# Kernel optimization log

Measured on AMD Instinct MI355X. Metric: run time of the kernel, lower is better.

Reference implementation:

```python
import jax, jax.numpy as jnp
import numpy as np

EPS = 1e-5

def _sqnorm(x):
    return jnp.sum(x * x, axis=-1, keepdims=True)

def _norm(x):
    return jnp.sqrt(_sqnorm(x) + 1e-15)

def _artanh(x):
    return jnp.arctanh(jnp.clip(x, -1.0 + EPS, 1.0 - EPS))

def exp0(v):
    n = _norm(v)
    return jnp.tanh(n) * v / jnp.maximum(n, EPS)

def log0(x):
    n = jnp.clip(_norm(x), EPS, 1.0 - EPS)
    return _artanh(n) * x / n

def mob_scalar(x, r):
    n = jnp.clip(_norm(x), EPS, 1.0 - EPS)
    return jnp.tanh(r * _artanh(n)) * x / n

def mob_add(x, y):
    x2 = _sqnorm(x); y2 = _sqnorm(y)
    xy = jnp.sum(x * y, axis=-1, keepdims=True)
    num = (1.0 + 2.0 * xy + y2) * x + (1.0 - x2) * y
    den = 1.0 + 2.0 * xy + x2 * y2
    return num / jnp.maximum(den, EPS)

def pdist(x, y):
    # Poincare-ball geodesic distance, keepdims on last axis
    d2 = _sqnorm(x - y)
    den = jnp.maximum((1.0 - _sqnorm(x)) * (1.0 - _sqnorm(y)), EPS)
    return jnp.arccosh(jnp.maximum(1.0 + 2.0 * d2 / den, 1.0 + 1e-7))

def _coattention(D, Q, q1):
    # vectorized form of the per-slot loop: each slot i reads the ORIGINAL D[:, i]
    Dd = jax.lax.stop_gradient(D)                       # Zk_s is detached in torch
    # [N, F_D, F_Q, 1] attention over Q neighbors for every D slot
    G = jax.nn.softmax(-pdist(Dd[:, :, None, :], Q[:, None, :, :]), axis=2)
    nh = exp0(jnp.sum(log0(mob_scalar(Q[:, None, :, :], G)), axis=2))  # [N, F_D, d]
    return mob_add(mob_scalar(Dd, q1), nh)

def _aggregate(h_self, h_neigh, scalar):
    att = jax.nn.softmax(-pdist(h_self[:, None, :], h_neigh), axis=1)  # [N, F, 1]
    nTE = exp0(jnp.sum(log0(mob_scalar(h_neigh, att)), axis=1))        # [N, d]
    return mob_add(mob_scalar(h_self, scalar), nTE)

def _mode_forward(x, D_idx, Q_idx, emb0, emb1, win, bin_, q, qq, q1, aw1, ab1, aw2, wout, bout):
    f = jnp.concatenate([emb0[x[:, 0]], emb1[x[:, 1]]], axis=-1)  # [N, 64]
    f = exp0(f @ win + bin_)
    D = f[D_idx]; Q = f[Q_idx]                                    # [N, F, d]
    h_neigh = _coattention(D, Q, q1)
    e1 = _aggregate(f, h_neigh, q)
    e2 = _aggregate(f, Q, qq)
    z = jnp.stack([log0(e1), log0(e2)], axis=1)                   # [N, 2, d]
    beta = jax.nn.softmax(jnp.tanh(z @ aw1 + ab1) @ aw2, axis=1)  # [N, 2, 1]
    rst = exp0(jnp.sum(beta * z, axis=1))
    return exp0(log0(rst) @ wout + bout)

N, F, DH, V0, V1 = 2048, 20, 64, 100000, 1000

def setup_inputs() -> dict:
    key = jax.random.key(0)
    ks = jax.random.split(key, 32)
    def mk(k, shape, s=0.1):
        return (jax.random.normal(k, shape) * s).astype(jnp.float32)
    inp = {
        'x': jax.random.randint(ks[0], (N, 2), 0, V1).astype(jnp.int32),
        'idx_sim': jax.random.randint(ks[1], (N, F), 0, N).astype(jnp.int32),
        'idx_cor': jax.random.randint(ks[2], (N, F), 0, N).astype(jnp.int32),
    }
    for mi, m in enumerate(['sim', 'cor']):
        kk = jax.random.split(ks[3 + mi], 12)
        inp[f'emb0_{m}'] = mk(kk[0], (V0, 32))
        inp[f'emb1_{m}'] = mk(kk[1], (V1, 32))
        inp[f'win_{m}'] = mk(kk[2], (64, DH))
        inp[f'bin_{m}'] = mk(kk[3], (DH,))
        inp[f'q_{m}'] = jnp.full((1,), 0.1, jnp.float32)
        inp[f'qq_{m}'] = jnp.full((1,), 0.1, jnp.float32)
        inp[f'q1_{m}'] = jnp.full((1,), 0.1, jnp.float32)
        inp[f'aw1_{m}'] = mk(kk[4], (64, 32))
        inp[f'ab1_{m}'] = mk(kk[5], (32,))
        inp[f'aw2_{m}'] = mk(kk[6], (32, 1))
        inp[f'wout_{m}'] = mk(kk[7], (DH, 64))
        inp[f'bout_{m}'] = mk(kk[8], (64,))
    return inp

def reference(x, idx_sim, idx_cor,
              emb0_sim, emb1_sim, win_sim, bin_sim, q_sim, qq_sim, q1_sim,
              aw1_sim, ab1_sim, aw2_sim, wout_sim, bout_sim,
              emb0_cor, emb1_cor, win_cor, bin_cor, q_cor, qq_cor, q1_cor,
              aw1_cor, ab1_cor, aw2_cor, wout_cor, bout_cor):
    # mode 'sim': D = feat[idx_cor], Q = feat[idx_sim]; mode 'cor': swapped
    out_sim = _mode_forward(x, idx_cor, idx_sim, emb0_sim, emb1_sim, win_sim, bin_sim,
                            q_sim, qq_sim, q1_sim, aw1_sim, ab1_sim, aw2_sim, wout_sim, bout_sim)
    out_cor = _mode_forward(x, idx_sim, idx_cor, emb0_cor, emb1_cor, win_cor, bin_cor,
                            q_cor, qq_cor, q1_cor, aw1_cor, ab1_cor, aw2_cor, wout_cor, bout_cor)
    return jnp.stack([out_sim, out_cor], axis=0)  # [2, N, 64]
```

## Files before the change

### kernel.cpp

```cpp
#include <hip/hip_runtime.h>

#define EPS 1e-5f
#define ONE_M_EPS (1.0f - 1e-5f)
#define NROW 2048
#define FF 20
#define DH 64
#define PADW (DH + 4)
#define PADH 72
#define NPAIR (FF * FF)
#define NPAIR2 (NPAIR + FF)

typedef float v2f __attribute__((ext_vector_type(2)));
typedef _Float16 v2h __attribute__((ext_vector_type(2)));

__device__ __forceinline__ float frcp(float x) { return __builtin_amdgcn_rcpf(x); }
__device__ __forceinline__ float fsq(float x) { return __builtin_amdgcn_sqrtf(x); }
__device__ __forceinline__ v2f pkfma(v2f a, v2f b, v2f c) {
  return __builtin_elementwise_fma(a, b, c);
}
__device__ __forceinline__ float rdlane(float v, int lane) {
  return __int_as_float(__builtin_amdgcn_readlane(__float_as_int(v), lane));
}

template <int CTRL>
__device__ __forceinline__ float dppadd(float x) {
  int t = __builtin_amdgcn_update_dpp(0, __float_as_int(x), CTRL, 0xf, 0xf, false);
  return x + __int_as_float(t);
}
__device__ __forceinline__ float wredb(float v) {
  v = dppadd<0x111>(v);
  v = dppadd<0x112>(v);
  v = dppadd<0x114>(v);
  v = dppadd<0x118>(v);
  v = dppadd<0x142>(v);
  v = dppadd<0x143>(v);
  return rdlane(v, 63);
}

__device__ __forceinline__ float ftanh(float x) {
  float ax = fabsf(x);
  float e = __expf(-2.f * ax);
  float t = (1.f - e) * frcp(1.f + e);
  return copysignf(t, x);
}

__device__ __forceinline__ float ftanhp(float x) {
  float e = __expf(-2.f * x);
  return (1.f - e) * frcp(1.f + e);
}

__device__ __forceinline__ float fatanh(float x) {
  return 0.5f * __logf((1.f + x) * frcp(1.f - x));
}

__device__ __forceinline__ float clampn(float x) {
  return fminf(fmaxf(x, EPS), ONE_M_EPS);
}

__device__ __forceinline__ float expnacosh(float arg) {
  return frcp(arg + fsq(fmaxf(arg * arg - 1.f, 0.f)));
}

__device__ __forceinline__ float dot64(const float* __restrict__ a,
                                       const float* __restrict__ b) {
  const float4* ap = (const float4*)a;
  const float4* bp = (const float4*)b;
  v2f accA = {0.f, 0.f}, accB = {0.f, 0.f};
#pragma unroll
  for (int kk = 0; kk < DH / 4; ++kk) {
    float4 x = ap[kk];
    float4 y = bp[kk];
    accA = pkfma(v2f{x.x, x.y}, v2f{y.x, y.y}, accA);
    accB = pkfma(v2f{x.z, x.w}, v2f{y.z, y.w}, accB);
  }
  v2f acc = accA + accB;
  return acc.x + acc.y;
}

__device__ __forceinline__ float dot64h(const _Float16* __restrict__ a,
                                        const _Float16* __restrict__ b) {
  const uint4* ap = (const uint4*)a;
  const uint4* bp = (const uint4*)b;
  float acc0 = 0.f, acc1 = 0.f;
#pragma unroll
  for (int kk = 0; kk < 8; ++kk) {
    uint4 x = ap[kk];
    uint4 y = bp[kk];
    acc0 = __builtin_amdgcn_fdot2(__builtin_bit_cast(v2h, x.x),
                                  __builtin_bit_cast(v2h, y.x), acc0, false);
    acc1 = __builtin_amdgcn_fdot2(__builtin_bit_cast(v2h, x.y),
                                  __builtin_bit_cast(v2h, y.y), acc1, false);
    acc0 = __builtin_amdgcn_fdot2(__builtin_bit_cast(v2h, x.z),
                                  __builtin_bit_cast(v2h, y.z), acc0, false);
    acc1 = __builtin_amdgcn_fdot2(__builtin_bit_cast(v2h, x.w),
                                  __builtin_bit_cast(v2h, y.w), acc1, false);
  }
  return acc0 + acc1;
}

struct FeatParams {
  const float *emb0, *emb1, *win, *bin;
  float* fout;
};

struct ModeParams {
  const float* f;
  const int *Didx, *Qidx;
  const float *q1p, *qp, *qqp, *aw1, *ab1, *aw2, *wout, *bout;
  float* out;
};

__global__ __launch_bounds__(64) void feat_kernel(const int* __restrict__ x,
                                                  FeatParams ps, FeatParams pc) {
  const int bid = blockIdx.x;
  const int mode = bid >= NROW;
  const FeatParams P = mode ? pc : ps;
  const int n = bid - mode * NROW;
  const int l = threadIdx.x;
  __shared__ float u[DH];
  int x0 = x[n * 2 + 0];
  int x1 = x[n * 2 + 1];
  u[l] = (l < 32) ? P.emb0[x0 * 32 + l] : P.emb1[x1 * 32 + (l - 32)];
  __syncthreads();
  v2f acc2 = {P.bin[l], 0.f};
#pragma unroll
  for (int k = 0; k < DH; k += 2) {
    v2f uv = *(const v2f*)&u[k];
    v2f wv = {P.win[k * DH + l], P.win[(k + 1) * DH + l]};
    acc2 = pkfma(uv, wv, acc2);
  }
  float acc = acc2.x + acc2.y;
  float a2 = wredb(acc * acc);
  float nn = fsq(a2 + 1e-15f);
  P.fout[n * DH + l] = ftanhp(nn) * frcp(fmaxf(nn, EPS)) * acc;
}

__global__ __launch_bounds__(256) void mode_kernel(ModeParams pm0,
                                                   ModeParams pm1) {
  const int bid = blockIdx.x;
  const int mode = bid >= NROW;
  const ModeParams P = mode ? pm1 : pm0;
  const int n = bid - mode * NROW;
  const int tid = threadIdx.x;
  const int l = tid & 63;
  const int w = tid >> 6;

  __shared__ alignas(16) float Ds[FF][PADW];
  __shared__ alignas(16) float Qs[FF][PADW];
  __shared__ alignas(16) float fs_[PADW];
  __shared__ alignas(16) _Float16 Dh[FF][PADH];
  __shared__ alignas(16) _Float16 Qh[FF][PADH];
  __shared__ alignas(16) _Float16 fh[PADH];
  __shared__ alignas(16) float Gm[NPAIR];
  __shared__ float Fq[FF];
  __shared__ float D2[FF];
  __shared__ float FD[FF], X2s[FF];
  __shared__ float Q2[FF], WQ[FF];
  __shared__ float C1[FF], C2[FF], WH[FF];
  __shared__ float zb[2][DH];
  __shared__ float ub[DH];

  float (*As)[PADW] = Qs;

  const float* f = P.f;
  float fv = f[n * DH + l];

  for (int i = w; i < FF; i += 4) {
    float dv = f[P.Didx[n * FF + i] * DH + l];
    float qv = f[P.Qidx[n * FF + i] * DH + l];
    Ds[i][l] = dv;
    Qs[i][l] = qv;
    Dh[i][l] = (_Float16)dv;
    Qh[i][l] = (_Float16)qv;
  }
  if (w == 0) {
    fs_[l] = fv;
    fh[l] = (_Float16)fv;
  }
  float f2 = wredb(fv * fv);
  float fnc = clampn(fsq(f2 + 1e-15f));
  float fA = fatanh(fnc);
  float q1 = P.q1p[0], qsc = P.qp[0], qqsc = P.qqp[0];
  __syncthreads();

  if (w < 2 && l < FF) {
    const float* rp = (w == 0) ? &Ds[l][0] : &Qs[l][0];
    float dot = dot64(rp, rp);
    float nc = clampn(fsq(dot + 1e-15f));
    float at = fatanh(nc);
    if (w == 0) {
      D2[l] = dot;
      float fd = ftanh(q1 * at) * frcp(nc);
      FD[l] = fd;
      X2s[l] = fd * fd * dot;
    } else {
      Q2[l] = dot;
      WQ[l] = at * frcp(nc);
    }
  }
  __syncthreads();

  float qregS[FF];
#pragma unroll
  for (int j = 0; j < FF; ++j) qregS[j] = WQ[j] * Qs[j][l];

  for (int p = tid; p < NPAIR2; p += 256) {
    int i = p / FF;
    int j = p - i * FF;
    const _Float16* ap = (i < FF) ? &Dh[i][0] : &fh[0];
    float dot = dot64h(ap, &Qh[j][0]);
    if (i < FF) {
      float d2 = D2[i] + Q2[j] - 2.f * dot;
      float den = fmaxf((1.f - D2[i]) * (1.f - Q2[j]), EPS);
      float arg = fmaxf(1.f + 2.f * d2 * frcp(den), 1.f + 1e-7f);
      Gm[p] = expnacosh(arg);
    } else {
      Fq[j] = dot;
    }
  }
  __syncthreads();

  float acc5[5];
#pragma unroll
  for (int s = 0; s < 5; ++s) {
    const int i = w + 4 * s;
    const float4* gr = (const float4*)(&Gm[i * FF]);
    v2f ss2 = {0.f, 0.f};
    v2f ac2 = {0.f, 0.f};
#pragma unroll
    for (int jq = 0; jq < FF / 4; ++jq) {
      float4 g4 = gr[jq];
      ss2 += v2f{g4.x, g4.y} + v2f{g4.z, g4.w};
      ac2 = pkfma(v2f{g4.x, g4.y}, v2f{qregS[4 * jq + 0], qregS[4 * jq + 1]},
                  ac2);
      ac2 = pkfma(v2f{g4.z, g4.w}, v2f{qregS[4 * jq + 2], qregS[4 * jq + 3]},
                  ac2);
    }
    float acc = (ac2.x + ac2.y) * frcp(ss2.x + ss2.y);
    acc5[s] = acc;
    As[i][l] = acc;
  }
  __syncthreads();

  if (w == 0) {
    const bool isA = (l < FF);
    const bool isX = (l >= 32 && l < 32 + FF);
    const float* pa = isA ? &As[l][0] : (isX ? &As[l - 32][0] : &fs_[0]);
    const float* pc2 = isA ? &As[l][0] : (isX ? &Ds[l - 32][0] : &fs_[0]);
    float dotv = dot64(pa, pc2);
    float xyv = __shfl(dotv, l + 32, 64);
    if (isA) {
      float a2 = dotv;
      float xy0 = xyv;
      float nn = fsq(a2 + 1e-15f);
      float ec = ftanhp(nn) * frcp(fmaxf(nn, EPS));
      float fDc = FD[l];
      float x2 = X2s[l];
      float y2 = ec * ec * a2;
      float xy = fDc * ec * xy0;
      float al = 1.f + 2.f * xy + y2;
      float be = 1.f - x2;
      float rd = frcp(fmaxf(1.f + 2.f * xy + x2 * y2, EPS));
      C1[l] = al * fDc * rd;
      C2[l] = be * ec * rd;
      float h2 = (al * al * x2 + 2.f * al * be * xy + be * be * y2) * rd * rd;
      D2[l] = h2;
      float nc = clampn(fsq(h2 + 1e-15f));
      WH[l] = fatanh(nc) * frcp(nc);
    }
  }
  __syncthreads();

#pragma unroll
  for (int s = 0; s < 5; ++s) {
    const int i = w + 4 * s;
    Ds[i][l] = fmaf(C1[i], Ds[i][l], C2[i] * acc5[s]);
  }
  __syncthreads();

  if (w < 2) {
    float a1 = 0.f;
    float wh = 1.f;
    if (w == 0) {
      if (l < FF) {
        float h2 = D2[l];
        wh = WH[l];
        float dot = dot64(&fs_[0], &Ds[l][0]);
        float d2 = f2 + h2 - 2.f * dot;
        float den = fmaxf((1.f - f2) * (1.f - h2), EPS);
        float arg = fmaxf(1.f + 2.f * d2 * frcp(den), 1.f + 1e-7f);
        a1 = expnacosh(arg);
      }
    } else {
      if (l < FF) {
        float d2 = f2 + Q2[l] - 2.f * Fq[l];
        float den = fmaxf((1.f - f2) * (1.f - Q2[l]), EPS);
        float arg = fmaxf(1.f + 2.f * d2 * frcp(den), 1.f + 1e-7f);
        a1 = expnacosh(arg);
      }
    }
    float s = wredb(a1);
    float c = (l < FF) ? a1 * frcp(s) * wh : 0.f;
    float accE = 0.f;
    if (w == 0) {
#pragma unroll
      for (int j = 0; j < FF; ++j) accE = fmaf(rdlane(c, j), Ds[j][l], accE);
    } else {
#pragma unroll
      for (int j = 0; j < FF; ++j) accE = fmaf(rdlane(c, j), qregS[j], accE);
    }
    float a2 = wredb(accE * accE);
    float nn = fsq(a2 + 1e-15f);
    float ec = ftanhp(nn) * frcp(fmaxf(nn, EPS));
    float nTE = ec * accE;
    float r = (w == 0) ? qsc : qqsc;
    float fsc = ftanh(r * fA) * frcp(fnc);
    float xv = fsc * fv;
    float x2 = fsc * fsc * f2;
    float y2 = ec * ec * a2;
    float xy = wredb(xv * nTE);
    float al = 1.f + 2.f * xy + y2;
    float be = 1.f - x2;
    float rd = frcp(fmaxf(1.f + 2.f * xy + x2 * y2, EPS));
    float ev = (al * xv + be * nTE) * rd;
    float es = (al * al * x2 + 2.f * al * be * xy + be * be * y2) * rd * rd;
    float n1 = clampn(fsq(es + 1e-15f));
    zb[w][l] = fatanh(n1) * frcp(n1) * ev;
  }
  __syncthreads();

  if (w == 0) {
    int p_ = l >> 5, c_ = l & 31;
    v2f mm2 = {P.ab1[c_], 0.f};
#pragma unroll
    for (int k = 0; k < DH; k += 2) {
      v2f zv = *(const v2f*)&zb[p_][k];
      v2f av = {P.aw1[k * 32 + c_], P.aw1[(k + 1) * 32 + c_]};
      mm2 = pkfma(zv, av, mm2);
    }
    float tt = ftanh(mm2.x + mm2.y);
    float sr = tt * P.aw2[c_];
    sr = dppadd<0x111>(sr);
    sr = dppadd<0x112>(sr);
    sr = dppadd<0x114>(sr);
    sr = dppadd<0x118>(sr);
    sr = dppadd<0x142>(sr);
    float s0 = rdlane(sr, 31);
    float s1 = rdlane(sr, 63);
    float bm = fmaxf(s0, s1);
    float b0 = __expf(s0 - bm), b1 = __expf(s1 - bm);
    float bi = frcp(b0 + b1);
    b0 *= bi;
    b1 *= bi;
    float rv = fmaf(b0, zb[0][l], b1 * zb[1][l]);
    float r2 = wredb(rv * rv);
    float rn = fsq(r2 + 1e-15f);
    float sc = ftanhp(rn) * frcp(fmaxf(rn, EPS));
    float rst = sc * rv;
    float rr = sc * sc * r2;
    float rc = clampn(fsq(rr + 1e-15f));
    ub[l] = fatanh(rc) * frcp(rc) * rst;
  }
  __syncthreads();

  if (w == 0) {
    v2f oo2 = {0.f, 0.f};
#pragma unroll
    for (int k = 0; k < DH; k += 2) {
      v2f uv = *(const v2f*)&ub[k];
      v2f wv = {P.wout[k * DH + l], P.wout[(k + 1) * DH + l]};
      oo2 = pkfma(uv, wv, oo2);
    }
    float oo = P.bout[l] + oo2.x + oo2.y;
    float o2 = wredb(oo * oo);
    float on = fsq(o2 + 1e-15f);
    P.out[n * DH + l] = ftanhp(on) * frcp(fmaxf(on, EPS)) * oo;
  }
}

extern "C" void kernel_launch(void* const* d_in, const int* in_sizes, int n_in,
                              void* d_out, int out_size, void* d_ws,
                              size_t ws_size, hipStream_t stream) {
  const int* x = (const int*)d_in[0];
  const int* idx_sim = (const int*)d_in[1];
  const int* idx_cor = (const int*)d_in[2];
  const float* p[2][12];
  for (int m = 0; m < 2; ++m)
    for (int k = 0; k < 12; ++k) p[m][k] = (const float*)d_in[3 + m * 12 + k];

  float* fsim = (float*)d_ws;
  float* fcor = fsim + NROW * DH;
  float* out = (float*)d_out;

  FeatParams fps = {p[0][0], p[0][1], p[0][2], p[0][3], fsim};
  FeatParams fpc = {p[1][0], p[1][1], p[1][2], p[1][3], fcor};
  feat_kernel<<<2 * NROW, 64, 0, stream>>>(x, fps, fpc);

  ModeParams m0 = {fsim, idx_cor, idx_sim, p[0][6], p[0][4], p[0][5],
                   p[0][7], p[0][8], p[0][9], p[0][10], p[0][11], out};
  ModeParams m1 = {fcor, idx_sim, idx_cor, p[1][6], p[1][4], p[1][5],
                   p[1][7], p[1][8], p[1][9], p[1][10], p[1][11], out + NROW * DH};
  mode_kernel<<<2 * NROW, 256, 0, stream>>>(m0, m1);
}
```

Before: 41.82 us.

## Store gathered neighbor rows only as fp16 and use fp16 dots for norms

Drops the fp32 shared copies of the D and Q neighbor rows and keeps only fp16 copies. Norms, the attention-output dots and Q register loads now read the fp16 data, and the coattention result is written to a new fp16 buffer. The mob_add cross term is computed from an unscaled dot that is issued right after the norm reduction, so the two wave reductions sit next to each other. This cuts shared-memory stores and footprint, which may allow higher occupancy, at the cost of fp16 precision in the norm computations near the ball boundary.

```diff
diff --git a/kernel.cpp b/kernel.cpp
--- a/kernel.cpp
+++ b/kernel.cpp
@@ -145,12 +145,12 @@
   const int l = tid & 63;
   const int w = tid >> 6;
 
-  __shared__ alignas(16) float Ds[FF][PADW];
-  __shared__ alignas(16) float Qs[FF][PADW];
+  __shared__ alignas(16) float Hs[FF][PADW];
   __shared__ alignas(16) float fs_[PADW];
   __shared__ alignas(16) _Float16 Dh[FF][PADH];
   __shared__ alignas(16) _Float16 Qh[FF][PADH];
   __shared__ alignas(16) _Float16 fh[PADH];
+  __shared__ alignas(16) _Float16 Ah[FF][PADH];
   __shared__ alignas(16) float Gm[NPAIR];
   __shared__ float Fq[FF];
   __shared__ float D2[FF];
@@ -160,16 +160,12 @@
   __shared__ float zb[2][DH];
   __shared__ float ub[DH];
 
-  float (*As)[PADW] = Qs;
-
   const float* f = P.f;
   float fv = f[n * DH + l];
 
   for (int i = w; i < FF; i += 4) {
     float dv = f[P.Didx[n * FF + i] * DH + l];
     float qv = f[P.Qidx[n * FF + i] * DH + l];
-    Ds[i][l] = dv;
-    Qs[i][l] = qv;
     Dh[i][l] = (_Float16)dv;
     Qh[i][l] = (_Float16)qv;
   }
@@ -184,8 +180,8 @@
   __syncthreads();
 
   if (w < 2 && l < FF) {
-    const float* rp = (w == 0) ? &Ds[l][0] : &Qs[l][0];
-    float dot = dot64(rp, rp);
+    const _Float16* rp = (w == 0) ? &Dh[l][0] : &Qh[l][0];
+    float dot = dot64h(rp, rp);
     float nc = clampn(fsq(dot + 1e-15f));
     float at = fatanh(nc);
     if (w == 0) {
@@ -202,7 +198,7 @@
 
   float qregS[FF];
 #pragma unroll
-  for (int j = 0; j < FF; ++j) qregS[j] = WQ[j] * Qs[j][l];
+  for (int j = 0; j < FF; ++j) qregS[j] = WQ[j] * (float)Qh[j][l];
 
   for (int p = tid; p < NPAIR2; p += 256) {
     int i = p / FF;
@@ -238,16 +234,16 @@
     }
     float acc = (ac2.x + ac2.y) * frcp(ss2.x + ss2.y);
     acc5[s] = acc;
-    As[i][l] = acc;
+    Ah[i][l] = (_Float16)acc;
   }
   __syncthreads();
 
   if (w == 0) {
     const bool isA = (l < FF);
     const bool isX = (l >= 32 && l < 32 + FF);
-    const float* pa = isA ? &As[l][0] : (isX ? &As[l - 32][0] : &fs_[0]);
-    const float* pc2 = isA ? &As[l][0] : (isX ? &Ds[l - 32][0] : &fs_[0]);
-    float dotv = dot64(pa, pc2);
+    const _Float16* pa = isA ? &Ah[l][0] : (isX ? &Ah[l - 32][0] : &fh[0]);
+    const _Float16* pb = isA ? &Ah[l][0] : (isX ? &Dh[l - 32][0] : &fh[0]);
+    float dotv = dot64h(pa, pb);
     float xyv = __shfl(dotv, l + 32, 64);
     if (isA) {
       float a2 = dotv;
@@ -274,7 +270,7 @@
 #pragma unroll
   for (int s = 0; s < 5; ++s) {
     const int i = w + 4 * s;
-    Ds[i][l] = fmaf(C1[i], Ds[i][l], C2[i] * acc5[s]);
+    Hs[i][l] = fmaf(C1[i], (float)Dh[i][l], C2[i] * acc5[s]);
   }
   __syncthreads();
 
@@ -285,7 +281,7 @@
       if (l < FF) {
         float h2 = D2[l];
         wh = WH[l];
-        float dot = dot64(&fs_[0], &Ds[l][0]);
+        float dot = dot64(&fs_[0], &Hs[l][0]);
         float d2 = f2 + h2 - 2.f * dot;
         float den = fmaxf((1.f - f2) * (1.f - h2), EPS);
         float arg = fmaxf(1.f + 2.f * d2 * frcp(den), 1.f + 1e-7f);
@@ -304,12 +300,13 @@
     float accE = 0.f;
     if (w == 0) {
 #pragma unroll
-      for (int j = 0; j < FF; ++j) accE = fmaf(rdlane(c, j), Ds[j][l], accE);
+      for (int j = 0; j < FF; ++j) accE = fmaf(rdlane(c, j), Hs[j][l], accE);
     } else {
 #pragma unroll
       for (int j = 0; j < FF; ++j) accE = fmaf(rdlane(c, j), qregS[j], accE);
     }
     float a2 = wredb(accE * accE);
+    float xy0w = wredb(fv * accE);
     float nn = fsq(a2 + 1e-15f);
     float ec = ftanhp(nn) * frcp(fmaxf(nn, EPS));
     float nTE = ec * accE;
@@ -318,7 +315,7 @@
     float xv = fsc * fv;
     float x2 = fsc * fsc * f2;
     float y2 = ec * ec * a2;
-    float xy = wredb(xv * nTE);
+    float xy = fsc * ec * xy0w;
     float al = 1.f + 2.f * xy + y2;
     float be = 1.f - x2;
     float rd = frcp(fmaxf(1.f + 2.f * xy + x2 * y2, EPS));
```

Measured after the change: 40.99 us. 1.02x faster.
